# Kernel tuning notes

Measured on AMD Instinct MI355X. Metric: run time of the kernel, lower is better.

## Reference

```python
import jax, jax.numpy as jnp
import numpy as np

V, K, C, F = 100000, 64, 3, 16
HID = [64, 64, 64]  # 'large' pca-net hidden widths (config.yaml stand-in)
EPS = 1e-4


def setup_inputs() -> dict:
    key = jax.random.key(0)
    ks = jax.random.split(key, 12)
    inp = {
        "coordinates": jax.random.normal(ks[0], (V, C), jnp.float32),
        "distsq": jax.random.uniform(ks[1], (V, K), jnp.float32),
        "features": jax.random.uniform(ks[2], (V, F), jnp.float32),
        "n_idxs": jax.random.randint(ks[3], (V, K), 0, V, jnp.int32),
    }
    dims = [C * C] + HID + [C * C]
    for i in range(len(dims) - 1):
        fan_in = dims[i]
        inp[f"W{i}"] = jax.random.normal(ks[4 + 2 * i], (dims[i], dims[i + 1]), jnp.float32) / np.sqrt(fan_in)
        inp[f"b{i}"] = jnp.zeros((dims[i + 1],), jnp.float32)
    return inp


def _neighbour_covariance(coordinates, distsq, features, n_idxs):
    # gather neighbour coords/features: [V,K,C], [V,K,F]
    nbc = jnp.take(coordinates, n_idxs, axis=0)
    nbf = jnp.take(features, n_idxs, axis=0)
    # per-neighbour per-feature weights, distsq pre-scaled by 10 in call()
    w = nbf * jnp.exp(-10.0 * distsq)[:, :, None]          # [V,K,F]
    wsum = jnp.sum(w, axis=1) + EPS                         # [V,F]
    mean = jnp.einsum("vkf,vkc->vfc", w, nbc) / wsum[:, :, None]  # [V,F,C]
    # E[x x^T] - mu mu^T (avoids materializing [V,K,F,C] centered diffs)
    m2 = jnp.einsum("vkf,vkc,vkd->vfcd", w, nbc, nbc) / wsum[:, :, None, None]
    cov = m2 - mean[:, :, :, None] * mean[:, :, None, :]    # [V,F,C,C]
    return cov, mean


def reference(coordinates, distsq, features, n_idxs,
              W0, b0, W1, b1, W2, b2, W3, b3):
    cov, mean = _neighbour_covariance(coordinates, distsq, features, n_idxs)
    x = cov.reshape(-1, C * C)                              # [V*F, C^2]
    # per-layer path: ELU on every layer, including the final one
    for Wl, bl in ((W0, b0), (W1, b1), (W2, b2), (W3, b3)):
        x = jax.nn.elu(x @ Wl + bl)
    return x.reshape(-1, F * C * C)                         # [V, F*C^2]
```

## Files before the change

kernel.cpp:

```cpp
#include <hip/hip_runtime.h>
#include <hip/hip_bf16.h>
#include <math.h>

#define NV 100000
#define NK 64
#define NF 16
#define EPS_W 1e-4f
#define ROWS_BYTES ((size_t)NV * 16 * 32)
#define C4_BYTES   ((size_t)NV * 16)
#define WS_NEED    ROWS_BYTES
#define WS_NEED_C4 (ROWS_BYTES + C4_BYTES)
#define GRID_MLP 2084

typedef __attribute__((ext_vector_type(8))) short bf16x8;
typedef __attribute__((ext_vector_type(4))) float f32x4;

__device__ __forceinline__ unsigned short bfu(float x) {
    return __builtin_bit_cast(unsigned short, (__bf16)x);
}
__device__ __forceinline__ unsigned int pk2(float lo, float hi) {
    float2 t; t.x = lo; t.y = hi;
    __hip_bfloat162 r = __float22bfloat162_rn(t);
    unsigned int u;
    __builtin_memcpy(&u, &r, 4);
    return u;
}
__device__ __forceinline__ float eluf(float x) {
    return x > 0.f ? x : __expf(x) - 1.f;
}

__global__ void prep_kernel(const float* __restrict__ coords, float4* __restrict__ c4) {
    int v = blockIdx.x * 256 + threadIdx.x;
    if (v < NV) {
        float4 r;
        r.x = coords[3 * v + 0];
        r.y = coords[3 * v + 1];
        r.z = coords[3 * v + 2];
        r.w = 0.f;
        c4[v] = r;
    }
}

template<bool C4>
__launch_bounds__(256)
__global__ void cov_kernel(const float* __restrict__ coords,
                           const float4* __restrict__ c4,
                           const float* __restrict__ distsq,
                           const float* __restrict__ feats,
                           const int*   __restrict__ nidx,
                           unsigned char* __restrict__ ws)
{
    __shared__ float sEW[16][64];
    __shared__ int   sIX[16][64];
    const int tid = threadIdx.x;
    const int gv  = tid >> 4;
    const int f   = tid & 15;
    const int v   = blockIdx.x * 16 + gv;

    {
        const size_t base = (size_t)v * NK + 4 * f;
        float4 d4 = *(const float4*)(distsq + base);
        int4   i4 = *(const int4*)(nidx + base);
        sEW[gv][4*f+0] = __expf(-10.f * d4.x);
        sEW[gv][4*f+1] = __expf(-10.f * d4.y);
        sEW[gv][4*f+2] = __expf(-10.f * d4.z);
        sEW[gv][4*f+3] = __expf(-10.f * d4.w);
        sIX[gv][4*f+0] = i4.x; sIX[gv][4*f+1] = i4.y;
        sIX[gv][4*f+2] = i4.z; sIX[gv][4*f+3] = i4.w;
    }
    __syncthreads();

    float s = 0.f, m0=0.f,m1=0.f,m2=0.f;
    float q00=0.f,q01=0.f,q02=0.f,q11=0.f,q12=0.f,q22=0.f;

    #pragma unroll 8
    for (int k = 0; k < NK; ++k) {
        int   idx = sIX[gv][k];
        float ew  = sEW[gv][k];
        float w   = feats[(size_t)idx * NF + f] * ew;
        float x, y, z;
        if constexpr (C4) {
            float4 cd = c4[idx];
            x = cd.x; y = cd.y; z = cd.z;
        } else {
            x = coords[(size_t)idx*3+0];
            y = coords[(size_t)idx*3+1];
            z = coords[(size_t)idx*3+2];
        }
        s += w;
        m0 = fmaf(w,x,m0); m1 = fmaf(w,y,m1); m2 = fmaf(w,z,m2);
        float wx=w*x, wy=w*y, wz=w*z;
        q00=fmaf(wx,x,q00); q01=fmaf(wx,y,q01); q02=fmaf(wx,z,q02);
        q11=fmaf(wy,y,q11); q12=fmaf(wy,z,q12); q22=fmaf(wz,z,q22);
    }
    float inv = 1.f / (s + EPS_W);
    float mu0=m0*inv, mu1=m1*inv, mu2=m2*inv;
    float c00=fmaf(-mu0,mu0,q00*inv);
    float c01=fmaf(-mu0,mu1,q01*inv);
    float c02=fmaf(-mu0,mu2,q02*inv);
    float c11=fmaf(-mu1,mu1,q11*inv);
    float c12=fmaf(-mu1,mu2,q12*inv);
    float c22=fmaf(-mu2,mu2,q22*inv);

    uint4 lo, hi;
    lo.x = pk2(c00, c01);
    lo.y = pk2(c02, c01);
    lo.z = pk2(c11, c12);
    lo.w = pk2(c02, c12);
    hi.x = pk2(c22, 1.0f);
    hi.y = 0u; hi.z = 0u; hi.w = 0u;

    uint4* dst = (uint4*)(ws + ((size_t)v * 16 + f) * 32);
    dst[0] = lo;
    dst[1] = hi;
}

__device__ __forceinline__ bf16x8 rdfrag(const short* hb, int c, int g, int kc) {
    int boff = ((kc << 6) + (g << 4)) ^ ((c & 7) << 4);
    return *(const bf16x8*)(hb + c * 64 + (boff >> 1));
}
__device__ __forceinline__ void wrH(short* hb, int c, int g, int t,
                                    unsigned int p01, unsigned int p23) {
    int boff = ((t << 5) + (g << 3)) ^ ((c & 7) << 4);
    uint2 val; val.x = p01; val.y = p23;
    *(uint2*)(hb + c * 64 + (boff >> 1)) = val;
}
__device__ __forceinline__ bf16x8 rdW(const short* sw, int c, int g, int t, int kc) {
    int byte = (t << 11) + (c << 7) + (kc << 6) + (g << 4);
    byte ^= (c & 7) << 4;
    return *(const bf16x8*)((const char*)sw + byte);
}

__launch_bounds__(256)
__global__ void mlp4_kernel(const unsigned char* __restrict__ ws,
                            const float* __restrict__ W0, const float* __restrict__ b0,
                            const float* __restrict__ W1, const float* __restrict__ b1,
                            const float* __restrict__ W2, const float* __restrict__ b2,
                            const float* __restrict__ W3, const float* __restrict__ b3,
                            float* __restrict__ out)
{
    __shared__ __align__(16) short sW1[4096];
    __shared__ __align__(16) short sW2[4096];
    __shared__ __align__(16) short hbuf[4][2][1024];

    const int tid  = threadIdx.x;
    const int wid  = tid >> 6;
    const int lane = tid & 63;
    const int c    = lane & 15;
    const int g    = lane >> 4;

    union U8 { short s[8]; bf16x8 v; };

    #pragma unroll
    for (int r = 0; r < 2; ++r) {
        int t = tid + r * 256;
        int j = t & 63, o = t >> 6;
        U8 u1, u2;
        #pragma unroll
        for (int i = 0; i < 8; ++i) {
            u1.s[i] = (short)bfu(W1[(8 * o + i) * 64 + j]);
            u2.s[i] = (short)bfu(W2[(8 * o + i) * 64 + j]);
        }
        int byte = ((j << 7) + (o << 4)) ^ ((j & 7) << 4);
        *(bf16x8*)((char*)sW1 + byte) = u1.v;
        *(bf16x8*)((char*)sW2 + byte) = u2.v;
    }
    __syncthreads();

    bf16x8 w0f[4], w3f[2];
    #pragma unroll
    for (int t = 0; t < 4; ++t) {
        U8 u;
        #pragma unroll
        for (int i = 0; i < 8; ++i) {
            int k = 8 * g + i;
            float val = 0.f;
            if (k < 9)       val = W0[k * 64 + 16 * t + c];
            else if (k == 9) val = b0[16 * t + c];
            u.s[i] = (short)bfu(val);
        }
        w0f[t] = u.v;
    }
    #pragma unroll
    for (int kc = 0; kc < 2; ++kc) {
        U8 u;
        #pragma unroll
        for (int i = 0; i < 8; ++i) {
            int k = 32 * kc + 8 * g + i;
            u.s[i] = (short)bfu(c < 9 ? W3[k * 9 + c] : 0.f);
        }
        w3f[kc] = u.v;
    }
    float b1v[16], b2v[16], b3v[4];
    #pragma unroll
    for (int t = 0; t < 4; ++t)
        #pragma unroll
        for (int r = 0; r < 4; ++r) {
            b1v[4 * t + r] = b1[16 * t + 4 * g + r];
            b2v[4 * t + r] = b2[16 * t + 4 * g + r];
        }
    #pragma unroll
    for (int r = 0; r < 4; ++r)
        b3v[r] = (4 * g + r < 9) ? b3[4 * g + r] : 0.f;

    short* hb0 = &hbuf[wid][0][0];
    short* hb1 = &hbuf[wid][1][0];

    const int npair  = NV / 2;
    const int stride = gridDim.x * 4;
    int p = blockIdx.x * 4 + wid;
    if (p >= npair) return;

    const unsigned char* wp = ws + (size_t)p * 1024 + (c << 5) + ((g & 1) << 4);
    const size_t wstep = (size_t)stride * 1024;
    float* op0 = out + (size_t)p * 288 + 9 * c + (g << 2);
    const size_t ostep = (size_t)stride * 288;

    bf16x8 bin0 = *(const bf16x8*)(wp);
    bf16x8 bin1 = *(const bf16x8*)(wp + 512);

    for (; p < npair; p += stride) {
        const unsigned char* wpn = (p + stride < npair) ? (wp + wstep) : wp;
        bf16x8 nb0 = *(const bf16x8*)(wpn);
        bf16x8 nb1 = *(const bf16x8*)(wpn + 512);

        f32x4 A0[4], A1[4];

        {
            #pragma unroll
            for (int t = 0; t < 4; ++t) {
                f32x4 z4 = {0.f, 0.f, 0.f, 0.f};
                A0[t] = __builtin_amdgcn_mfma_f32_16x16x32_bf16(w0f[t], bin0, z4, 0, 0, 0);
                A1[t] = __builtin_amdgcn_mfma_f32_16x16x32_bf16(w0f[t], bin1, z4, 0, 0, 0);
            }
            #pragma unroll
            for (int t = 0; t < 4; ++t) {
                wrH(hb0, c, g, t, pk2(eluf(A0[t][0]), eluf(A0[t][1])),
                                  pk2(eluf(A0[t][2]), eluf(A0[t][3])));
                wrH(hb1, c, g, t, pk2(eluf(A1[t][0]), eluf(A1[t][1])),
                                  pk2(eluf(A1[t][2]), eluf(A1[t][3])));
            }
        }
        __asm__ volatile("s_waitcnt lgkmcnt(0)" ::: "memory");

        {
            bf16x8 h00 = rdfrag(hb0, c, g, 0), h01 = rdfrag(hb0, c, g, 1);
            bf16x8 h10 = rdfrag(hb1, c, g, 0), h11 = rdfrag(hb1, c, g, 1);
            #pragma unroll
            for (int t = 0; t < 4; ++t) {
                bf16x8 wa = rdW(sW1, c, g, t, 0);
                bf16x8 wb = rdW(sW1, c, g, t, 1);
                f32x4 a0 = { b1v[4*t+0], b1v[4*t+1], b1v[4*t+2], b1v[4*t+3] };
                f32x4 a1 = a0;
                a0 = __builtin_amdgcn_mfma_f32_16x16x32_bf16(wa, h00, a0, 0, 0, 0);
                a0 = __builtin_amdgcn_mfma_f32_16x16x32_bf16(wb, h01, a0, 0, 0, 0);
                a1 = __builtin_amdgcn_mfma_f32_16x16x32_bf16(wa, h10, a1, 0, 0, 0);
                a1 = __builtin_amdgcn_mfma_f32_16x16x32_bf16(wb, h11, a1, 0, 0, 0);
                A0[t] = a0; A1[t] = a1;
            }
            #pragma unroll
            for (int t = 0; t < 4; ++t) {
                wrH(hb0, c, g, t, pk2(eluf(A0[t][0]), eluf(A0[t][1])),
                                  pk2(eluf(A0[t][2]), eluf(A0[t][3])));
                wrH(hb1, c, g, t, pk2(eluf(A1[t][0]), eluf(A1[t][1])),
                                  pk2(eluf(A1[t][2]), eluf(A1[t][3])));
            }
        }
        __asm__ volatile("s_waitcnt lgkmcnt(0)" ::: "memory");

        {
            bf16x8 h00 = rdfrag(hb0, c, g, 0), h01 = rdfrag(hb0, c, g, 1);
            bf16x8 h10 = rdfrag(hb1, c, g, 0), h11 = rdfrag(hb1, c, g, 1);
            #pragma unroll
            for (int t = 0; t < 4; ++t) {
                bf16x8 wa = rdW(sW2, c, g, t, 0);
                bf16x8 wb = rdW(sW2, c, g, t, 1);
                f32x4 a0 = { b2v[4*t+0], b2v[4*t+1], b2v[4*t+2], b2v[4*t+3] };
                f32x4 a1 = a0;
                a0 = __builtin_amdgcn_mfma_f32_16x16x32_bf16(wa, h00, a0, 0, 0, 0);
                a0 = __builtin_amdgcn_mfma_f32_16x16x32_bf16(wb, h01, a0, 0, 0, 0);
                a1 = __builtin_amdgcn_mfma_f32_16x16x32_bf16(wa, h10, a1, 0, 0, 0);
                a1 = __builtin_amdgcn_mfma_f32_16x16x32_bf16(wb, h11, a1, 0, 0, 0);
                A0[t] = a0; A1[t] = a1;
            }
            #pragma unroll
            for (int t = 0; t < 4; ++t) {
                wrH(hb0, c, g, t, pk2(eluf(A0[t][0]), eluf(A0[t][1])),
                                  pk2(eluf(A0[t][2]), eluf(A0[t][3])));
                wrH(hb1, c, g, t, pk2(eluf(A1[t][0]), eluf(A1[t][1])),
                                  pk2(eluf(A1[t][2]), eluf(A1[t][3])));
            }
        }
        __asm__ volatile("s_waitcnt lgkmcnt(0)" ::: "memory");

        {
            bf16x8 h00 = rdfrag(hb0, c, g, 0), h01 = rdfrag(hb0, c, g, 1);
            bf16x8 h10 = rdfrag(hb1, c, g, 0), h11 = rdfrag(hb1, c, g, 1);
            f32x4 a0 = { b3v[0], b3v[1], b3v[2], b3v[3] };
            f32x4 a1 = a0;
            a0 = __builtin_amdgcn_mfma_f32_16x16x32_bf16(w3f[0], h00, a0, 0, 0, 0);
            a0 = __builtin_amdgcn_mfma_f32_16x16x32_bf16(w3f[1], h01, a0, 0, 0, 0);
            a1 = __builtin_amdgcn_mfma_f32_16x16x32_bf16(w3f[0], h10, a1, 0, 0, 0);
            a1 = __builtin_amdgcn_mfma_f32_16x16x32_bf16(w3f[1], h11, a1, 0, 0, 0);
            float* op1 = op0 + 144;
            if (g < 2) {
                op0[0] = eluf(a0[0]); op0[1] = eluf(a0[1]);
                op0[2] = eluf(a0[2]); op0[3] = eluf(a0[3]);
                op1[0] = eluf(a1[0]); op1[1] = eluf(a1[1]);
                op1[2] = eluf(a1[2]); op1[3] = eluf(a1[3]);
            } else if (g == 2) {
                op0[0] = eluf(a0[0]);
                op1[0] = eluf(a1[0]);
            }
        }

        bin0 = nb0; bin1 = nb1;
        wp = wpn;
        op0 += ostep;
    }
}

__launch_bounds__(256, 2)
__global__ void fused_pca_mlp(const float* __restrict__ coords,
                              const float* __restrict__ distsq,
                              const float* __restrict__ feats,
                              const int*   __restrict__ nidx,
                              const float* __restrict__ W0, const float* __restrict__ b0,
                              const float* __restrict__ W1, const float* __restrict__ b1,
                              const float* __restrict__ W2, const float* __restrict__ b2,
                              const float* __restrict__ W3, const float* __restrict__ b3,
                              float* __restrict__ out)
{
    __shared__ __align__(16) float sW0t[64 * 9];
    __shared__ __align__(16) float sW1t[64 * 64];
    __shared__ __align__(16) float sW2t[64 * 64];
    __shared__ __align__(16) float sW3t[9 * 64];
    __shared__ float sB0[64], sB1[64], sB2[64], sB3[9];
    const int tid = threadIdx.x;
    for (int t = tid; t < 64 * 9; t += 256) { int j = t / 9, i = t - j * 9; sW0t[t] = W0[i * 64 + j]; }
    for (int t = tid; t < 64 * 64; t += 256) { int j = t >> 6, i = t & 63; sW1t[t] = W1[i * 64 + j]; }
    for (int t = tid; t < 64 * 64; t += 256) { int j = t >> 6, i = t & 63; sW2t[t] = W2[i * 64 + j]; }
    for (int t = tid; t < 9 * 64; t += 256) { int j = t >> 6, i = t & 63; sW3t[t] = W3[i * 9 + j]; }
    if (tid < 64) { sB0[tid] = b0[tid]; sB1[tid] = b1[tid]; sB2[tid] = b2[tid]; }
    if (tid < 9)  { sB3[tid] = b3[tid]; }
    __syncthreads();
    const int g = tid >> 4, f = tid & 15;
    const int v = blockIdx.x * 16 + g;
    if (v >= NV) return;
    const int* nix = nidx + (size_t)v * NK;
    const float* dsq = distsq + (size_t)v * NK;
    float s = 0.f, m0=0,m1=0,m2=0, q00=0,q01=0,q02=0,q11=0,q12=0,q22=0;
    #pragma unroll 4
    for (int k = 0; k < NK; ++k) {
        int idx = nix[k];
        float ew = __expf(-10.0f * dsq[k]);
        float w = feats[(size_t)idx * NF + f] * ew;
        float x = coords[(size_t)idx*3+0], y = coords[(size_t)idx*3+1], z = coords[(size_t)idx*3+2];
        s += w; m0 = fmaf(w,x,m0); m1 = fmaf(w,y,m1); m2 = fmaf(w,z,m2);
        float wx=w*x, wy=w*y, wz=w*z;
        q00=fmaf(wx,x,q00); q01=fmaf(wx,y,q01); q02=fmaf(wx,z,q02);
        q11=fmaf(wy,y,q11); q12=fmaf(wy,z,q12); q22=fmaf(wz,z,q22);
    }
    float inv = 1.0f/(s+EPS_W), mu0=m0*inv, mu1=m1*inv, mu2=m2*inv;
    float xr[9];
    xr[0]=fmaf(-mu0,mu0,q00*inv); xr[1]=fmaf(-mu0,mu1,q01*inv); xr[2]=fmaf(-mu0,mu2,q02*inv);
    xr[3]=xr[1]; xr[4]=fmaf(-mu1,mu1,q11*inv); xr[5]=fmaf(-mu1,mu2,q12*inv);
    xr[6]=xr[2]; xr[7]=xr[5]; xr[8]=fmaf(-mu2,mu2,q22*inv);
    float h[64], gg[64];
    #pragma unroll
    for (int j = 0; j < 64; ++j) {
        float aa = sB0[j]; const float* wr = sW0t + j * 9;
        #pragma unroll
        for (int i = 0; i < 9; ++i) aa = fmaf(xr[i], wr[i], aa);
        h[j] = eluf(aa);
    }
    #pragma unroll
    for (int j = 0; j < 64; ++j) {
        float aa = sB1[j]; const float4* wr = (const float4*)(sW1t + (j << 6));
        #pragma unroll
        for (int i4 = 0; i4 < 16; ++i4) { float4 wv = wr[i4];
            aa = fmaf(h[4*i4+0],wv.x,aa); aa = fmaf(h[4*i4+1],wv.y,aa);
            aa = fmaf(h[4*i4+2],wv.z,aa); aa = fmaf(h[4*i4+3],wv.w,aa); }
        gg[j] = eluf(aa);
    }
    #pragma unroll
    for (int j = 0; j < 64; ++j) {
        float aa = sB2[j]; const float4* wr = (const float4*)(sW2t + (j << 6));
        #pragma unroll
        for (int i4 = 0; i4 < 16; ++i4) { float4 wv = wr[i4];
            aa = fmaf(gg[4*i4+0],wv.x,aa); aa = fmaf(gg[4*i4+1],wv.y,aa);
            aa = fmaf(gg[4*i4+2],wv.z,aa); aa = fmaf(gg[4*i4+3],wv.w,aa); }
        h[j] = eluf(aa);
    }
    float o[9];
    #pragma unroll
    for (int j = 0; j < 9; ++j) {
        float aa = sB3[j]; const float4* wr = (const float4*)(sW3t + (j << 6));
        #pragma unroll
        for (int i4 = 0; i4 < 16; ++i4) { float4 wv = wr[i4];
            aa = fmaf(h[4*i4+0],wv.x,aa); aa = fmaf(h[4*i4+1],wv.y,aa);
            aa = fmaf(h[4*i4+2],wv.z,aa); aa = fmaf(h[4*i4+3],wv.w,aa); }
        o[j] = eluf(aa);
    }
    float* op = out + ((size_t)v * NF + f) * 9;
    #pragma unroll
    for (int j = 0; j < 9; ++j) op[j] = o[j];
}

extern "C" void kernel_launch(void* const* d_in, const int* in_sizes, int n_in,
                              void* d_out, int out_size, void* d_ws, size_t ws_size,
                              hipStream_t stream) {
    (void)in_sizes; (void)n_in; (void)out_size;
    const float* coords = (const float*)d_in[0];
    const float* distsq = (const float*)d_in[1];
    const float* feats  = (const float*)d_in[2];
    const int*   nidx   = (const int*)d_in[3];
    const float* W0 = (const float*)d_in[4];
    const float* b0 = (const float*)d_in[5];
    const float* W1 = (const float*)d_in[6];
    const float* b1 = (const float*)d_in[7];
    const float* W2 = (const float*)d_in[8];
    const float* b2 = (const float*)d_in[9];
    const float* W3 = (const float*)d_in[10];
    const float* b3 = (const float*)d_in[11];
    float* out = (float*)d_out;

    if (ws_size >= WS_NEED_C4) {
        unsigned char* ws = (unsigned char*)d_ws;
        float4* c4 = (float4*)(ws + ROWS_BYTES);
        hipLaunchKernelGGL(prep_kernel, dim3((NV + 255) / 256), dim3(256), 0, stream,
                           coords, c4);
        hipLaunchKernelGGL((cov_kernel<true>), dim3(NV / 16), dim3(256), 0, stream,
                           coords, c4, distsq, feats, nidx, ws);
        hipLaunchKernelGGL(mlp4_kernel, dim3(GRID_MLP), dim3(256), 0, stream,
                           ws, W0, b0, W1, b1, W2, b2, W3, b3, out);
    } else if (ws_size >= WS_NEED) {
        unsigned char* ws = (unsigned char*)d_ws;
        hipLaunchKernelGGL((cov_kernel<false>), dim3(NV / 16), dim3(256), 0, stream,
                           coords, (const float4*)nullptr, distsq, feats, nidx, ws);
        hipLaunchKernelGGL(mlp4_kernel, dim3(GRID_MLP), dim3(256), 0, stream,
                           ws, W0, b0, W1, b1, W2, b2, W3, b3, out);
    } else {
        hipLaunchKernelGGL(fused_pca_mlp, dim3(NV / 16), dim3(256), 0, stream,
                           coords, distsq, feats, nidx,
                           W0, b0, W1, b1, W2, b2, W3, b3, out);
    }
}
```

Baseline: 220.4 us.

## Gather bf16 feature copy in covariance kernel and simplify MLP to one vertex per wave

A prep kernel now also writes a bf16 copy of the features, and the covariance kernel gathers that half-size copy instead of the fp32 features, cutting random-gather traffic. The MLP kernel processes one vertex per wave iteration instead of two, drops the explicit LDS waitcnt barriers, halves its LDS hidden buffer, requests 4 blocks per CU, and raises the grid size. Rounding features to bf16 before weighting adds precision loss, and the single-vertex loop gives less MFMA interleaving per iteration in exchange for higher occupancy.

```diff
diff --git a/kernel.cpp b/kernel.cpp
--- a/kernel.cpp
+++ b/kernel.cpp
@@ -8,9 +8,10 @@
 #define EPS_W 1e-4f
 #define ROWS_BYTES ((size_t)NV * 16 * 32)
 #define C4_BYTES   ((size_t)NV * 16)
+#define FB_BYTES   ((size_t)NV * 16 * 2)
 #define WS_NEED    ROWS_BYTES
-#define WS_NEED_C4 (ROWS_BYTES + C4_BYTES)
-#define GRID_MLP 2084
+#define WS_NEED2   (ROWS_BYTES + C4_BYTES + FB_BYTES)
+#define GRID_MLP 3125
 
 typedef __attribute__((ext_vector_type(8))) short bf16x8;
 typedef __attribute__((ext_vector_type(4))) float f32x4;
@@ -29,7 +30,10 @@
     return x > 0.f ? x : __expf(x) - 1.f;
 }
 
-__global__ void prep_kernel(const float* __restrict__ coords, float4* __restrict__ c4) {
+__global__ void prep2_kernel(const float* __restrict__ coords,
+                             const float* __restrict__ feats,
+                             float4* __restrict__ c4,
+                             unsigned short* __restrict__ fb) {
     int v = blockIdx.x * 256 + threadIdx.x;
     if (v < NV) {
         float4 r;
@@ -38,13 +42,18 @@
         r.z = coords[3 * v + 2];
         r.w = 0.f;
         c4[v] = r;
-    }
-}
-
-template<bool C4>
+        const float* fp = feats + (size_t)v * 16;
+        unsigned short* op = fb + (size_t)v * 16;
+        #pragma unroll
+        for (int i = 0; i < 16; ++i) op[i] = bfu(fp[i]);
+    }
+}
+
+template<int MODE>
 __launch_bounds__(256)
 __global__ void cov_kernel(const float* __restrict__ coords,
                            const float4* __restrict__ c4,
+                           const unsigned short* __restrict__ fb,
                            const float* __restrict__ distsq,
                            const float* __restrict__ feats,
                            const int*   __restrict__ nidx,
@@ -77,16 +86,19 @@
     for (int k = 0; k < NK; ++k) {
         int   idx = sIX[gv][k];
         float ew  = sEW[gv][k];
-        float w   = feats[(size_t)idx * NF + f] * ew;
-        float x, y, z;
-        if constexpr (C4) {
+        float ft, x, y, z;
+        if constexpr (MODE == 2) {
+            unsigned int fu = fb[(size_t)idx * NF + f];
+            ft = __builtin_bit_cast(float, fu << 16);
             float4 cd = c4[idx];
             x = cd.x; y = cd.y; z = cd.z;
         } else {
+            ft = feats[(size_t)idx * NF + f];
             x = coords[(size_t)idx*3+0];
             y = coords[(size_t)idx*3+1];
             z = coords[(size_t)idx*3+2];
         }
+        float w = ft * ew;
         s += w;
         m0 = fmaf(w,x,m0); m1 = fmaf(w,y,m1); m2 = fmaf(w,z,m2);
         float wx=w*x, wy=w*y, wz=w*z;
@@ -131,8 +143,8 @@
     return *(const bf16x8*)((const char*)sw + byte);
 }
 
-__launch_bounds__(256)
-__global__ void mlp4_kernel(const unsigned char* __restrict__ ws,
+__launch_bounds__(256, 4)
+__global__ void mlp5_kernel(const unsigned char* __restrict__ ws,
                             const float* __restrict__ W0, const float* __restrict__ b0,
                             const float* __restrict__ W1, const float* __restrict__ b1,
                             const float* __restrict__ W2, const float* __restrict__ b2,
@@ -141,7 +153,7 @@
 {
     __shared__ __align__(16) short sW1[4096];
     __shared__ __align__(16) short sW2[4096];
-    __shared__ __align__(16) short hbuf[4][2][1024];
+    __shared__ __align__(16) short hbuf[4][1024];
 
     const int tid  = threadIdx.x;
     const int wid  = tid >> 6;
@@ -203,120 +215,85 @@
     for (int r = 0; r < 4; ++r)
         b3v[r] = (4 * g + r < 9) ? b3[4 * g + r] : 0.f;
 
-    short* hb0 = &hbuf[wid][0][0];
-    short* hb1 = &hbuf[wid][1][0];
-
-    const int npair  = NV / 2;
+    short* hb = &hbuf[wid][0];
+
     const int stride = gridDim.x * 4;
-    int p = blockIdx.x * 4 + wid;
-    if (p >= npair) return;
-
-    const unsigned char* wp = ws + (size_t)p * 1024 + (c << 5) + ((g & 1) << 4);
-    const size_t wstep = (size_t)stride * 1024;
-    float* op0 = out + (size_t)p * 288 + 9 * c + (g << 2);
-    const size_t ostep = (size_t)stride * 288;
-
-    bf16x8 bin0 = *(const bf16x8*)(wp);
-    bf16x8 bin1 = *(const bf16x8*)(wp + 512);
-
-    for (; p < npair; p += stride) {
-        const unsigned char* wpn = (p + stride < npair) ? (wp + wstep) : wp;
-        bf16x8 nb0 = *(const bf16x8*)(wpn);
-        bf16x8 nb1 = *(const bf16x8*)(wpn + 512);
-
-        f32x4 A0[4], A1[4];
+    int v = blockIdx.x * 4 + wid;
+    if (v >= NV) return;
+
+    const unsigned char* wp = ws + (size_t)v * 512 + (c << 5) + ((g & 1) << 4);
+    const size_t wstep = (size_t)stride * 512;
+    float* op = out + (size_t)v * 144 + 9 * c + (g << 2);
+    const size_t ostep = (size_t)stride * 144;
+
+    bf16x8 bin = *(const bf16x8*)(wp);
+
+    for (; v < NV; v += stride) {
+        const unsigned char* wpn = (v + stride < NV) ? (wp + wstep) : wp;
+        bf16x8 nb = *(const bf16x8*)(wpn);
+
+        f32x4 A[4];
+
+        #pragma unroll
+        for (int t = 0; t < 4; ++t) {
+            f32x4 z4 = {0.f, 0.f, 0.f, 0.f};
+            A[t] = __builtin_amdgcn_mfma_f32_16x16x32_bf16(w0f[t], bin, z4, 0, 0, 0);
+        }
+        #pragma unroll
+        for (int t = 0; t < 4; ++t)
+            wrH(hb, c, g, t, pk2(eluf(A[t][0]), eluf(A[t][1])),
+                             pk2(eluf(A[t][2]), eluf(A[t][3])));
 
         {
-            #pragma unroll
-            for (int t = 0; t < 4; ++t) {
-                f32x4 z4 = {0.f, 0.f, 0.f, 0.f};
-                A0[t] = __builtin_amdgcn_mfma_f32_16x16x32_bf16(w0f[t], bin0, z4, 0, 0, 0);
-                A1[t] = __builtin_amdgcn_mfma_f32_16x16x32_bf16(w0f[t], bin1, z4, 0, 0, 0);
-            }
-            #pragma unroll
-            for (int t = 0; t < 4; ++t) {
-                wrH(hb0, c, g, t, pk2(eluf(A0[t][0]), eluf(A0[t][1])),
-                                  pk2(eluf(A0[t][2]), eluf(A0[t][3])));
-                wrH(hb1, c, g, t, pk2(eluf(A1[t][0]), eluf(A1[t][1])),
-                                  pk2(eluf(A1[t][2]), eluf(A1[t][3])));
-            }
-        }
-        __asm__ volatile("s_waitcnt lgkmcnt(0)" ::: "memory");
-
-        {
-            bf16x8 h00 = rdfrag(hb0, c, g, 0), h01 = rdfrag(hb0, c, g, 1);
-            bf16x8 h10 = rdfrag(hb1, c, g, 0), h11 = rdfrag(hb1, c, g, 1);
+            bf16x8 h0 = rdfrag(hb, c, g, 0), h1 = rdfrag(hb, c, g, 1);
             #pragma unroll
             for (int t = 0; t < 4; ++t) {
                 bf16x8 wa = rdW(sW1, c, g, t, 0);
                 bf16x8 wb = rdW(sW1, c, g, t, 1);
-                f32x4 a0 = { b1v[4*t+0], b1v[4*t+1], b1v[4*t+2], b1v[4*t+3] };
-                f32x4 a1 = a0;
-                a0 = __builtin_amdgcn_mfma_f32_16x16x32_bf16(wa, h00, a0, 0, 0, 0);
-                a0 = __builtin_amdgcn_mfma_f32_16x16x32_bf16(wb, h01, a0, 0, 0, 0);
-                a1 = __builtin_amdgcn_mfma_f32_16x16x32_bf16(wa, h10, a1, 0, 0, 0);
-                a1 = __builtin_amdgcn_mfma_f32_16x16x32_bf16(wb, h11, a1, 0, 0, 0);
-                A0[t] = a0; A1[t] = a1;
+                f32x4 a = { b1v[4*t+0], b1v[4*t+1], b1v[4*t+2], b1v[4*t+3] };
+                a = __builtin_amdgcn_mfma_f32_16x16x32_bf16(wa, h0, a, 0, 0, 0);
+                a = __builtin_amdgcn_mfma_f32_16x16x32_bf16(wb, h1, a, 0, 0, 0);
+                A[t] = a;
             }
             #pragma unroll
-            for (int t = 0; t < 4; ++t) {
-                wrH(hb0, c, g, t, pk2(eluf(A0[t][0]), eluf(A0[t][1])),
-                                  pk2(eluf(A0[t][2]), eluf(A0[t][3])));
-                wrH(hb1, c, g, t, pk2(eluf(A1[t][0]), eluf(A1[t][1])),
-                                  pk2(eluf(A1[t][2]), eluf(A1[t][3])));
-            }
-        }
-        __asm__ volatile("s_waitcnt lgkmcnt(0)" ::: "memory");
+            for (int t = 0; t < 4; ++t)
+                wrH(hb, c, g, t, pk2(eluf(A[t][0]), eluf(A[t][1])),
+                                 pk2(eluf(A[t][2]), eluf(A[t][3])));
+        }
 
         {
-            bf16x8 h00 = rdfrag(hb0, c, g, 0), h01 = rdfrag(hb0, c, g, 1);
-            bf16x8 h10 = rdfrag(hb1, c, g, 0), h11 = rdfrag(hb1, c, g, 1);
+            bf16x8 h0 = rdfrag(hb, c, g, 0), h1 = rdfrag(hb, c, g, 1);
             #pragma unroll
             for (int t = 0; t < 4; ++t) {
                 bf16x8 wa = rdW(sW2, c, g, t, 0);
                 bf16x8 wb = rdW(sW2, c, g, t, 1);
-                f32x4 a0 = { b2v[4*t+0], b2v[4*t+1], b2v[4*t+2], b2v[4*t+3] };
-                f32x4 a1 = a0;
-                a0 = __builtin_amdgcn_mfma_f32_16x16x32_bf16(wa, h00, a0, 0, 0, 0);
-                a0 = __builtin_amdgcn_mfma_f32_16x16x32_bf16(wb, h01, a0, 0, 0, 0);
-                a1 = __builtin_amdgcn_mfma_f32_16x16x32_bf16(wa, h10, a1, 0, 0, 0);
-                a1 = __builtin_amdgcn_mfma_f32_16x16x32_bf16(wb, h11, a1, 0, 0, 0);
-                A0[t] = a0; A1[t] = a1;
+                f32x4 a = { b2v[4*t+0], b2v[4*t+1], b2v[4*t+2], b2v[4*t+3] };
+                a = __builtin_amdgcn_mfma_f32_16x16x32_bf16(wa, h0, a, 0, 0, 0);
+                a = __builtin_amdgcn_mfma_f32_16x16x32_bf16(wb, h1, a, 0, 0, 0);
+                A[t] = a;
             }
             #pragma unroll
-            for (int t = 0; t < 4; ++t) {
-                wrH(hb0, c, g, t, pk2(eluf(A0[t][0]), eluf(A0[t][1])),
-                                  pk2(eluf(A0[t][2]), eluf(A0[t][3])));
-                wrH(hb1, c, g, t, pk2(eluf(A1[t][0]), eluf(A1[t][1])),
-                                  pk2(eluf(A1[t][2]), eluf(A1[t][3])));
+            for (int t = 0; t < 4; ++t)
+                wrH(hb, c, g, t, pk2(eluf(A[t][0]), eluf(A[t][1])),
+                                 pk2(eluf(A[t][2]), eluf(A[t][3])));
+        }
+
+        {
+            bf16x8 h0 = rdfrag(hb, c, g, 0), h1 = rdfrag(hb, c, g, 1);
+            f32x4 a = { b3v[0], b3v[1], b3v[2], b3v[3] };
+            a = __builtin_amdgcn_mfma_f32_16x16x32_bf16(w3f[0], h0, a, 0, 0, 0);
+            a = __builtin_amdgcn_mfma_f32_16x16x32_bf16(w3f[1], h1, a, 0, 0, 0);
+            if (g < 2) {
+                op[0] = eluf(a[0]); op[1] = eluf(a[1]);
+                op[2] = eluf(a[2]); op[3] = eluf(a[3]);
+            } else if (g == 2) {
+                op[0] = eluf(a[0]);
             }
         }
-        __asm__ volatile("s_waitcnt lgkmcnt(0)" ::: "memory");
-
-        {
-            bf16x8 h00 = rdfrag(hb0, c, g, 0), h01 = rdfrag(hb0, c, g, 1);
-            bf16x8 h10 = rdfrag(hb1, c, g, 0), h11 = rdfrag(hb1, c, g, 1);
-            f32x4 a0 = { b3v[0], b3v[1], b3v[2], b3v[3] };
-            f32x4 a1 = a0;
-            a0 = __builtin_amdgcn_mfma_f32_16x16x32_bf16(w3f[0], h00, a0, 0, 0, 0);
-            a0 = __builtin_amdgcn_mfma_f32_16x16x32_bf16(w3f[1], h01, a0, 0, 0, 0);
-            a1 = __builtin_amdgcn_mfma_f32_16x16x32_bf16(w3f[0], h10, a1, 0, 0, 0);
-            a1 = __builtin_amdgcn_mfma_f32_16x16x32_bf16(w3f[1], h11, a1, 0, 0, 0);
-            float* op1 = op0 + 144;
-            if (g < 2) {
-                op0[0] = eluf(a0[0]); op0[1] = eluf(a0[1]);
-                op0[2] = eluf(a0[2]); op0[3] = eluf(a0[3]);
-                op1[0] = eluf(a1[0]); op1[1] = eluf(a1[1]);
-                op1[2] = eluf(a1[2]); op1[3] = eluf(a1[3]);
-            } else if (g == 2) {
-                op0[0] = eluf(a0[0]);
-                op1[0] = eluf(a1[0]);
-            }
-        }
-
-        bin0 = nb0; bin1 = nb1;
+
+        bin = nb;
         wp = wpn;
-        op0 += ostep;
+        op += ostep;
     }
 }
 
@@ -425,20 +402,22 @@
     const float* b3 = (const float*)d_in[11];
     float* out = (float*)d_out;
 
-    if (ws_size >= WS_NEED_C4) {
+    if (ws_size >= WS_NEED2) {
         unsigned char* ws = (unsigned char*)d_ws;
         float4* c4 = (float4*)(ws + ROWS_BYTES);
-        hipLaunchKernelGGL(prep_kernel, dim3((NV + 255) / 256), dim3(256), 0, stream,
-                           coords, c4);
-        hipLaunchKernelGGL((cov_kernel<true>), dim3(NV / 16), dim3(256), 0, stream,
-                           coords, c4, distsq, feats, nidx, ws);
-        hipLaunchKernelGGL(mlp4_kernel, dim3(GRID_MLP), dim3(256), 0, stream,
+        unsigned short* fb = (unsigned short*)(ws + ROWS_BYTES + C4_BYTES);
+        hipLaunchKernelGGL(prep2_kernel, dim3((NV + 255) / 256), dim3(256), 0, stream,
+                           coords, feats, c4, fb);
+        hipLaunchKernelGGL((cov_kernel<2>), dim3(NV / 16), dim3(256), 0, stream,
+                           coords, c4, fb, distsq, feats, nidx, ws);
+        hipLaunchKernelGGL(mlp5_kernel, dim3(GRID_MLP), dim3(256), 0, stream,
                            ws, W0, b0, W1, b1, W2, b2, W3, b3, out);
     } else if (ws_size >= WS_NEED) {
         unsigned char* ws = (unsigned char*)d_ws;
-        hipLaunchKernelGGL((cov_kernel<false>), dim3(NV / 16), dim3(256), 0, stream,
-                           coords, (const float4*)nullptr, distsq, feats, nidx, ws);
-        hipLaunchKernelGGL(mlp4_kernel, dim3(GRID_MLP), dim3(256), 0, stream,
+        hipLaunchKernelGGL((cov_kernel<0>), dim3(NV / 16), dim3(256), 0, stream,
+                           coords, (const float4*)nullptr, (const unsigned short*)nullptr,
+                           distsq, feats, nidx, ws);
+        hipLaunchKernelGGL(mlp5_kernel, dim3(GRID_MLP), dim3(256), 0, stream,
                            ws, W0, b0, W1, b1, W2, b2, W3, b3, out);
     } else {
         hipLaunchKernelGGL(fused_pca_mlp, dim3(NV / 16), dim3(256), 0, stream,
```

Result: slower. 302.5 us (+37.3%).
